# Performance work log

Hardware: AMD Instinct MI355X
Metric: run time of the kernel (lower is better)

## Reference

```python
import jax, jax.numpy as jnp
import numpy as np

B, S, D, H, HID = 4, 1024, 1024, 16, 4096
DK = D // H
EPS = 1e-6


def _ln(x):
    # LayerNorm without affine, eps=1e-6
    mu = jnp.mean(x, axis=-1, keepdims=True)
    var = jnp.var(x, axis=-1, keepdims=True)
    return (x - mu) / jnp.sqrt(var + EPS)


def _lin(x, W, b):
    # torch Linear convention: W is [out, in]
    y = jnp.einsum('...i,oi->...o', x, W)
    return y + b if b is not None else y


def setup_inputs() -> dict:
    key = jax.random.key(0)
    ks = jax.random.split(key, 16)
    sc = lambda fan_in: 1.0 / np.sqrt(fan_in)
    inp = {
        'x': jax.random.normal(ks[0], (B, S, D), jnp.float32),
        'cond': jax.random.normal(ks[1], (B, 1, D), jnp.float32),
        'Wq': jax.random.normal(ks[2], (D, D), jnp.float32) * sc(D),
        'bq': jnp.zeros((D,), jnp.float32),
        'Wk': jax.random.normal(ks[3], (D, D), jnp.float32) * sc(D),
        'bk': jnp.zeros((D,), jnp.float32),
        'Wv': jax.random.normal(ks[4], (D, D), jnp.float32) * sc(D),
        'bv': jnp.zeros((D,), jnp.float32),
        'Wo': jax.random.normal(ks[5], (D, D), jnp.float32) * sc(D),
        'bo': jnp.zeros((D,), jnp.float32),
        'W1': jax.random.normal(ks[6], (HID, D), jnp.float32) * sc(D),
        'b1': jnp.zeros((HID,), jnp.float32),
        'W2': jax.random.normal(ks[7], (D, HID), jnp.float32) * sc(HID),
        'b2': jnp.zeros((D,), jnp.float32),
        'Wada': jax.random.normal(ks[8], (6 * D, D), jnp.float32) * sc(D),
        'bada': jnp.zeros((6 * D,), jnp.float32),
    }
    return inp


def reference(x, cond, Wq, bq, Wk, bk, Wv, bv, Wo, bo, W1, b1, W2, b2, Wada, bada):
    # adaLN modulation: SiLU -> Linear -> chunk 6 along last dim
    mod = _lin(jax.nn.silu(cond), Wada, bada)  # [B,1,6D]
    gama1, beta1, alpha1, gama2, beta2, alpha2 = jnp.split(mod, 6, axis=-1)

    # attention branch
    residual = x
    h = _ln(x) * (1.0 + beta1) + gama1  # modulate(shift=gama1, scale=beta1)
    q = _lin(h, Wq, bq).reshape(B, S, H, DK)
    k = _lin(h, Wk, bk).reshape(B, S, H, DK)
    v = _lin(h, Wv, bv).reshape(B, S, H, DK)
    scores = jnp.einsum('bqhd,bkhd->bhqk', q, k) / jnp.sqrt(jnp.float32(DK))
    probs = jax.nn.softmax(scores, axis=-1)
    attn = jnp.einsum('bhqk,bkhd->bqhd', probs, v).reshape(B, S, D)
    attn = _lin(attn, Wo, bo)
    x = residual + alpha1 * attn

    # MLP branch
    residual = x
    h = _ln(x) * (1.0 + beta2) + gama2
    h = _lin(h, W1, b1)
    h = jax.nn.gelu(h, approximate=False)  # torch nn.GELU default (erf)
    h = _lin(h, W2, b2)
    return residual + alpha2 * h
```

## Files before the change

### kernel.cpp

```cpp
#include <hip/hip_runtime.h>
#include <cstdint>

typedef __bf16 bf16_t;
typedef __bf16 bf16x4 __attribute__((ext_vector_type(4)));
typedef __bf16 bf16x8 __attribute__((ext_vector_type(8)));
typedef float f32x4 __attribute__((ext_vector_type(4)));

#define B_ 4
#define S_ 1024
#define D_ 1024
#define HID_ 4096
#define MEG (1u << 20)

static const size_t OFF_WBF  = 0;
static const size_t OFF_BQKV = 25165824;
static const size_t OFF_MOD  = 25178112;
static const size_t OFF_H    = 25276416;
static const size_t OFF_QKV  = 33665024;
static const size_t OFF_VT   = 58830848;
static const size_t OFF_ATTN = 67219456;
static const size_t OFF_X1   = 75608064;
static const size_t OFF_PART = 92385280;
static const size_t OFF_MLPH = 159494144;

__device__ __forceinline__ void async_copy16(const bf16_t* g, bf16_t* l) {
  __builtin_amdgcn_global_load_lds(
      (__attribute__((address_space(1))) void*)(g),
      (__attribute__((address_space(3))) void*)(l), 16, 0, 0);
}

__global__ __launch_bounds__(256) void convert_pack(
    const float* __restrict__ Wq, const float* __restrict__ Wk,
    const float* __restrict__ Wv, const float* __restrict__ Wo,
    const float* __restrict__ W1, const float* __restrict__ W2,
    const float* __restrict__ bq, const float* __restrict__ bk,
    const float* __restrict__ bv, bf16_t* __restrict__ wbf,
    float* __restrict__ bqkv) {
  const int y = blockIdx.y;
  if (y == 6) {
    int i = blockIdx.x * 256 + threadIdx.x;
    if (i < 3072)
      bqkv[i] = i < 1024 ? bq[i] : (i < 2048 ? bk[i - 1024] : bv[i - 2048]);
    return;
  }
  const float* src; bf16_t* dst; int n;
  switch (y) {
    case 0: src = Wq; dst = wbf;           n = MEG;     break;
    case 1: src = Wk; dst = wbf + MEG;     n = MEG;     break;
    case 2: src = Wv; dst = wbf + 2*MEG;   n = MEG;     break;
    case 3: src = Wo; dst = wbf + 3*MEG;   n = MEG;     break;
    case 4: src = W1; dst = wbf + 4*MEG;   n = 4*MEG;   break;
    default: src = W2; dst = wbf + 8*MEG;  n = 4*MEG;   break;
  }
  int idx = (blockIdx.x * 256 + threadIdx.x) * 4;
  if (idx < n) {
    float4 v = *(const float4*)(src + idx);
    bf16x4 pk;
    pk.x = (__bf16)v.x; pk.y = (__bf16)v.y; pk.z = (__bf16)v.z; pk.w = (__bf16)v.w;
    *(bf16x4*)(dst + idx) = pk;
  }
}

__global__ __launch_bounds__(256) void ada_mod(
    const float* __restrict__ cond, const float* __restrict__ Wada,
    const float* __restrict__ bada, float* __restrict__ mod) {
  const int wave = threadIdx.x >> 6, lane = threadIdx.x & 63;
  const int o = blockIdx.x * 4 + wave;
  const float* wr = Wada + (size_t)o * D_;
  float a0 = 0.f, a1 = 0.f, a2 = 0.f, a3 = 0.f;
#pragma unroll
  for (int l = 0; l < 16; l++) {
    int i = l * 64 + lane;
    float w = wr[i];
    float c0 = cond[i], c1 = cond[1024 + i], c2 = cond[2048 + i], c3 = cond[3072 + i];
    a0 += w * (c0 / (1.0f + __expf(-c0)));
    a1 += w * (c1 / (1.0f + __expf(-c1)));
    a2 += w * (c2 / (1.0f + __expf(-c2)));
    a3 += w * (c3 / (1.0f + __expf(-c3)));
  }
#pragma unroll
  for (int offs = 32; offs; offs >>= 1) {
    a0 += __shfl_xor(a0, offs);
    a1 += __shfl_xor(a1, offs);
    a2 += __shfl_xor(a2, offs);
    a3 += __shfl_xor(a3, offs);
  }
  if (lane == 0) {
    float bb = bada[o];
    mod[o]          = a0 + bb;
    mod[6144 + o]   = a1 + bb;
    mod[12288 + o]  = a2 + bb;
    mod[18432 + o]  = a3 + bb;
  }
}

__global__ __launch_bounds__(256) void ln_modulate(
    const float* __restrict__ X, const float* __restrict__ mod,
    bf16_t* __restrict__ H, int goff) {
  const int row = blockIdx.x;
  const int b = row >> 10;
  const int t = threadIdx.x;
  const float* xr = X + (size_t)row * D_;
  float4 xv = *(const float4*)(xr + t * 4);
  float s = xv.x + xv.y + xv.z + xv.w;
  float q = xv.x*xv.x + xv.y*xv.y + xv.z*xv.z + xv.w*xv.w;
  const int wave = t >> 6, lane = t & 63;
#pragma unroll
  for (int offs = 32; offs; offs >>= 1) {
    s += __shfl_down(s, offs);
    q += __shfl_down(q, offs);
  }
  __shared__ float sb[4][2];
  if (lane == 0) { sb[wave][0] = s; sb[wave][1] = q; }
  __syncthreads();
  float st = sb[0][0] + sb[1][0] + sb[2][0] + sb[3][0];
  float qt = sb[0][1] + sb[1][1] + sb[2][1] + sb[3][1];
  float mu = st * (1.0f / D_);
  float var = qt * (1.0f / D_) - mu * mu;
  float rstd = rsqrtf(var + 1e-6f);
  const float* mb = mod + (size_t)b * 6144 + goff;
  const int c = t * 4;
  float4 gm = *(const float4*)(mb + c);
  float4 bt = *(const float4*)(mb + 1024 + c);
  bf16x4 pk;
  pk.x = (__bf16)((xv.x - mu) * rstd * (1.0f + bt.x) + gm.x);
  pk.y = (__bf16)((xv.y - mu) * rstd * (1.0f + bt.y) + gm.y);
  pk.z = (__bf16)((xv.z - mu) * rstd * (1.0f + bt.z) + gm.z);
  pk.w = (__bf16)((xv.w - mu) * rstd * (1.0f + bt.w) + gm.w);
  *(bf16x4*)(H + (size_t)row * D_ + c) = pk;
}

__global__ __launch_bounds__(256) void transpose_v(
    const bf16_t* __restrict__ qkv, bf16_t* __restrict__ vT) {
  __shared__ bf16_t tile[64][65];
  const int bh = blockIdx.y;
  const int b = bh >> 4, hh = bh & 15;
  const int s0 = blockIdx.x * 64;
  const int t = threadIdx.x;
  const int tx = t & 63, ty = t >> 6;
  const bf16_t* src = qkv + (size_t)b * S_ * 3072 + 2048 + hh * 64;
  for (int r = ty; r < 64; r += 4)
    tile[r][tx] = src[(size_t)(s0 + r) * 3072 + tx];
  __syncthreads();
  bf16_t* dst = vT + (size_t)bh * 64 * 1024;
  for (int r = ty; r < 64; r += 4)
    dst[(size_t)r * 1024 + s0 + tx] = tile[tx][r];
}

__global__ __launch_bounds__(256) void flash_attn(
    const bf16_t* __restrict__ qkv, const bf16_t* __restrict__ vT,
    bf16_t* __restrict__ attn) {
  __shared__ __align__(16) bf16_t Ks[2][2][64 * 64];
  __shared__ __align__(16) bf16_t Vs[2][2][64 * 64];
  __shared__ __align__(16) bf16_t Ps[4][2][16 * 64];

  const int t = threadIdx.x;
  const int wave = t >> 6, lane = t & 63;
  const int lm = lane & 15, quad = lane >> 4;
  const int bh = blockIdx.y;
  const int b = bh >> 4, hh = bh & 15;
  const int s0 = blockIdx.x * 64;

  const bf16_t* qbase = qkv + (size_t)b * S_ * 3072 + hh * 64;
  const bf16_t* kbase = qbase + 1024;
  const bf16_t* vbase = vT + (size_t)bh * (64 * 1024);

  const int row0 = t >> 3;
  const int cg = (t & 7) ^ (row0 & 7);
  const int o0 = t * 8, o1 = 2048 + t * 8;
  const bf16_t* kr = kbase + (size_t)row0 * 3072 + cg * 8;
  const bf16_t* vr0 = vbase + (size_t)row0 * 1024 + cg * 8;
  const bf16_t* vr1 = vbase + (size_t)(32 + row0) * 1024 + cg * 8;

  async_copy16(qbase + (size_t)(s0 + row0) * 3072 + cg * 8, &Ks[1][0][o0]);
  async_copy16(qbase + (size_t)(s0 + 32 + row0) * 3072 + cg * 8, &Ks[1][0][o1]);
  async_copy16(kr, &Ks[0][0][o0]);
  async_copy16(kr + (size_t)32 * 3072, &Ks[0][0][o1]);
  async_copy16(kr + (size_t)64 * 3072, &Ks[0][1][o0]);
  async_copy16(kr + (size_t)96 * 3072, &Ks[0][1][o1]);
  async_copy16(vr0, &Vs[0][0][o0]);
  async_copy16(vr1, &Vs[0][0][o1]);
  async_copy16(vr0 + 64, &Vs[0][1][o0]);
  async_copy16(vr1 + 64, &Vs[0][1][o1]);
  __syncthreads();

  bf16x8 aq0, aq1;
  {
    const int rq = wave * 16 + lm;
    const int rbq = lm & 7;
    aq0 = *(const bf16x8*)&Ks[1][0][rq * 64 + (quad ^ rbq) * 8];
    aq1 = *(const bf16x8*)&Ks[1][0][rq * 64 + ((4 + quad) ^ rbq) * 8];
  }
  __syncthreads();

  f32x4 accO[4] = {};
  float mrow[4], lrow[4];
#pragma unroll
  for (int r = 0; r < 4; r++) { mrow[r] = -1e30f; lrow[r] = 0.f; }

  const float SC = 0.18033688f;
  const int rb = lm & 7;

  for (int tt = 0; tt < 8; ++tt) {
    const int cur = tt & 1;
    if (tt < 7) {
      const int nb = cur ^ 1;
      const size_t k0n = (size_t)(tt + 1) << 7;
      const bf16_t* kn = kr + k0n * 3072;
      async_copy16(kn, &Ks[nb][0][o0]);
      async_copy16(kn + (size_t)32 * 3072, &Ks[nb][0][o1]);
      async_copy16(kn + (size_t)64 * 3072, &Ks[nb][1][o0]);
      async_copy16(kn + (size_t)96 * 3072, &Ks[nb][1][o1]);
      async_copy16(vr0 + k0n, &Vs[nb][0][o0]);
      async_copy16(vr1 + k0n, &Vs[nb][0][o1]);
      async_copy16(vr0 + k0n + 64, &Vs[nb][1][o0]);
      async_copy16(vr1 + k0n + 64, &Vs[nb][1][o1]);
    }

    f32x4 accS[8];
#pragma unroll
    for (int j = 0; j < 8; j++) accS[j] = (f32x4){0.f, 0.f, 0.f, 0.f};
    __builtin_amdgcn_s_setprio(1);
#pragma unroll
    for (int h = 0; h < 2; h++) {
#pragma unroll
      for (int ni = 0; ni < 4; ni++) {
        const int rk = ni * 16 + lm;
        bf16x8 b0 = *(const bf16x8*)&Ks[cur][h][rk * 64 + ((quad ^ rb)) * 8];
        bf16x8 b1 = *(const bf16x8*)&Ks[cur][h][rk * 64 + (((4 + quad) ^ rb)) * 8];
        f32x4 a = accS[h * 4 + ni];
        a = __builtin_amdgcn_mfma_f32_16x16x32_bf16(aq0, b0, a, 0, 0, 0);
        a = __builtin_amdgcn_mfma_f32_16x16x32_bf16(aq1, b1, a, 0, 0, 0);
        accS[h * 4 + ni] = a;
      }
    }
    __builtin_amdgcn_s_setprio(0);

    float mx[4];
#pragma unroll
    for (int r = 0; r < 4; r++) {
      float m0 = fmaxf(fmaxf(accS[0][r], accS[1][r]), fmaxf(accS[2][r], accS[3][r]));
      float m1 = fmaxf(fmaxf(accS[4][r], accS[5][r]), fmaxf(accS[6][r], accS[7][r]));
      float m8 = fmaxf(m0, m1);
      m8 = fmaxf(m8, __shfl_xor(m8, 1));
      m8 = fmaxf(m8, __shfl_xor(m8, 2));
      m8 = fmaxf(m8, __shfl_xor(m8, 4));
      m8 = fmaxf(m8, __shfl_xor(m8, 8));
      mx[r] = m8 * SC;
    }
    bool ok = (mx[0] - mrow[0] <= 8.0f) && (mx[1] - mrow[1] <= 8.0f) &&
              (mx[2] - mrow[2] <= 8.0f) && (mx[3] - mrow[3] <= 8.0f);
    if (!__all(ok)) {
#pragma unroll
      for (int r = 0; r < 4; r++) {
        float mnew = fmaxf(mrow[r], mx[r]);
        float al = exp2f(mrow[r] - mnew);
        mrow[r] = mnew;
        lrow[r] *= al;
#pragma unroll
        for (int di = 0; di < 4; di++) accO[di][r] *= al;
      }
    }
#pragma unroll
    for (int r = 0; r < 4; r++) {
      float sum = 0.f;
#pragma unroll
      for (int j = 0; j < 8; j++) {
        float p = exp2f(accS[j][r] * SC - mrow[r]);
        accS[j][r] = p;
        sum += p;
      }
      sum += __shfl_xor(sum, 1);
      sum += __shfl_xor(sum, 2);
      sum += __shfl_xor(sum, 4);
      sum += __shfl_xor(sum, 8);
      lrow[r] += sum;
    }

#pragma unroll
    for (int j = 0; j < 8; j++)
#pragma unroll
      for (int r = 0; r < 4; r++) {
        int prow = quad * 4 + r;
        int c = (j & 3) * 16 + lm;
        Ps[wave][j >> 2][prow * 64 + (((c >> 3) ^ (prow & 7)) << 3) + (c & 7)] =
            (__bf16)accS[j][r];
      }

    __builtin_amdgcn_s_setprio(1);
#pragma unroll
    for (int ks = 0; ks < 4; ks++) {
      const int half = ks >> 1, loc = ks & 1;
      bf16x8 ap = *(const bf16x8*)&Ps[wave][half]
          [lm * 64 + (((loc * 4 + quad) ^ rb)) * 8];
#pragma unroll
      for (int di = 0; di < 4; di++) {
        const int rv = di * 16 + lm;
        bf16x8 vv = *(const bf16x8*)&Vs[cur][half]
            [rv * 64 + (((loc * 4 + quad) ^ rb)) * 8];
        accO[di] = __builtin_amdgcn_mfma_f32_16x16x32_bf16(ap, vv, accO[di], 0, 0, 0);
      }
    }
    __builtin_amdgcn_s_setprio(0);
    __syncthreads();
  }

#pragma unroll
  for (int r = 0; r < 4; r++) {
    float inv = 1.0f / lrow[r];
    int prow = quad * 4 + r;
#pragma unroll
    for (int di = 0; di < 4; di++) {
      int col = di * 16 + lm;
      int cph = (col >> 3) ^ (prow & 7);
      Ps[wave][0][prow * 64 + cph * 8 + (col & 7)] = (__bf16)(accO[di][r] * inv);
    }
  }
  bf16_t* abase = attn + (size_t)b * S_ * 1024 +
                  (size_t)(s0 + wave * 16) * 1024 + hh * 64;
#pragma unroll
  for (int it = 0; it < 2; it++) {
    int slot = it * 64 + lane;
    int orow = slot >> 3;
    int gc = slot & 7;
    int cph = gc ^ (orow & 7);
    bf16x8 val = *(const bf16x8*)&Ps[wave][0][orow * 64 + cph * 8];
    *(bf16x8*)(abase + (size_t)orow * 1024 + gc * 8) = val;
  }
}

template <int EPI>
__global__ __launch_bounds__(256) void gemm_bt(
    const bf16_t* __restrict__ A, int lda, long long sAz,
    const bf16_t* __restrict__ B, int ldb, long long sBz,
    void* __restrict__ Cv, int ldc, long long sCz,
    int M, int N, int K,
    const float* __restrict__ bias,
    float scale) {
  __shared__ __align__(16) bf16_t As[2][128 * 32];
  __shared__ __align__(16) bf16_t Bs[2][128 * 32];

  const int z = blockIdx.z;
  A += (size_t)z * sAz;
  B += (size_t)z * sBz;

  {
    int d = blockIdx.x + gridDim.x * blockIdx.y;
    int xcd = d & 7, sId = d >> 3;
    int qq = sId & 31, panel = sId >> 5;
    const int bx = panel * 8 + (qq >> 2);
    const int by = xcd * 4 + (qq & 3);
    const int t = threadIdx.x;
    const int wave = t >> 6;
    const int lane = t & 63;
    const int lm = lane & 15;
    const int quad = lane >> 4;
    const int wr = wave >> 1;
    const int wc = wave & 1;

    const int m0 = by * 128;
    const int n0 = bx * 128;

    f32x4 acc[4][4] = {};

    const int srow = t >> 2;
    const int gch = (t & 3) ^ ((srow >> 1) & 3);
    const int lds_off = t * 8;
    const bf16_t* Ap0 = A + (size_t)(m0 + srow) * lda + gch * 8;
    const bf16_t* Ap1 = A + (size_t)(m0 + 64 + srow) * lda + gch * 8;
    const bf16_t* Bp0 = B + (size_t)(n0 + srow) * ldb + gch * 8;
    const bf16_t* Bp1 = B + (size_t)(n0 + 64 + srow) * ldb + gch * 8;

    const int sOff = (quad ^ ((lm >> 1) & 3)) * 8;

    const int niter = K >> 5;
    async_copy16(Ap0, &As[0][lds_off]);
    async_copy16(Ap1, &As[0][2048 + lds_off]);
    async_copy16(Bp0, &Bs[0][lds_off]);
    async_copy16(Bp1, &Bs[0][2048 + lds_off]);

    for (int it = 0; it < niter; ++it) {
      asm volatile("s_waitcnt vmcnt(0)\n\ts_barrier" ::: "memory");
      if (it + 1 < niter) {
        const int ko = (it + 1) << 5;
        const int nb = (it + 1) & 1;
        async_copy16(Ap0 + ko, &As[nb][lds_off]);
        async_copy16(Ap1 + ko, &As[nb][2048 + lds_off]);
        async_copy16(Bp0 + ko, &Bs[nb][lds_off]);
        async_copy16(Bp1 + ko, &Bs[nb][2048 + lds_off]);
      }
      const int cb = it & 1;
      bf16x8 af[4], bfr[4];
#pragma unroll
      for (int i = 0; i < 4; i++) {
        af[i] = *(const bf16x8*)&As[cb][(wr * 64 + i * 16 + lm) * 32 + sOff];
        bfr[i] = *(const bf16x8*)&Bs[cb][(wc * 64 + i * 16 + lm) * 32 + sOff];
      }
#pragma unroll
      for (int mi = 0; mi < 4; mi++)
#pragma unroll
        for (int ni = 0; ni < 4; ni++)
          acc[mi][ni] = __builtin_amdgcn_mfma_f32_16x16x32_bf16(
              af[mi], bfr[ni], acc[mi][ni], 0, 0, 0);
    }

    const size_t cz = (size_t)z * sCz;
#pragma unroll
    for (int mi = 0; mi < 4; mi++) {
#pragma unroll
      for (int ni = 0; ni < 4; ni++) {
#pragma unroll
        for (int r = 0; r < 4; r++) {
          int row = m0 + wr * 64 + mi * 16 + quad * 4 + r;
          int col = n0 + wc * 64 + ni * 16 + lm;
          float v = acc[mi][ni][r];
          size_t idx = cz + (size_t)row * ldc + col;
          if (EPI == 1) {
            ((float*)Cv)[idx] = v * scale;
          } else if (EPI == 0) {
            if (bias) v += bias[col];
            ((bf16_t*)Cv)[idx] = (__bf16)v;
          } else if (EPI == 3) {
            v += bias[col];
            float u = 1.5957691216f * (v + 0.044715f * v * v * v);
            float g = v / (1.0f + __expf(-u));
            ((bf16_t*)Cv)[idx] = (__bf16)g;
          }
        }
      }
    }
  }
}

__global__ __launch_bounds__(256) void reduce_ln(
    const float* __restrict__ part, const float* __restrict__ x,
    const float* __restrict__ bo, const float* __restrict__ mod,
    float* __restrict__ x1, bf16_t* __restrict__ h) {
  const int row = blockIdx.x;
  const int b = row >> 10;
  const int t = threadIdx.x;
  const int c = t * 4;
  const size_t idx = (size_t)row * 1024 + c;
  float4 p0 = *(const float4*)(part + idx);
  float4 p1 = *(const float4*)(part + 4194304 + idx);
  float4 bb = *(const float4*)(bo + c);
  float4 al = *(const float4*)(mod + (size_t)b * 6144 + 2048 + c);
  float4 xs = *(const float4*)(x + idx);
  float4 xv;
  xv.x = xs.x + al.x * (p0.x + p1.x + bb.x);
  xv.y = xs.y + al.y * (p0.y + p1.y + bb.y);
  xv.z = xs.z + al.z * (p0.z + p1.z + bb.z);
  xv.w = xs.w + al.w * (p0.w + p1.w + bb.w);
  *(float4*)(x1 + idx) = xv;

  float s = xv.x + xv.y + xv.z + xv.w;
  float q = xv.x*xv.x + xv.y*xv.y + xv.z*xv.z + xv.w*xv.w;
  const int wave = t >> 6, lane = t & 63;
#pragma unroll
  for (int offs = 32; offs; offs >>= 1) {
    s += __shfl_down(s, offs);
    q += __shfl_down(q, offs);
  }
  __shared__ float sb[4][2];
  if (lane == 0) { sb[wave][0] = s; sb[wave][1] = q; }
  __syncthreads();
  float st = sb[0][0] + sb[1][0] + sb[2][0] + sb[3][0];
  float qt = sb[0][1] + sb[1][1] + sb[2][1] + sb[3][1];
  float mu = st * (1.0f / D_);
  float var = qt * (1.0f / D_) - mu * mu;
  float rstd = rsqrtf(var + 1e-6f);
  const float* mb = mod + (size_t)b * 6144 + 3072;
  float4 gm = *(const float4*)(mb + c);
  float4 bt = *(const float4*)(mb + 1024 + c);
  bf16x4 pk;
  pk.x = (__bf16)((xv.x - mu) * rstd * (1.0f + bt.x) + gm.x);
  pk.y = (__bf16)((xv.y - mu) * rstd * (1.0f + bt.y) + gm.y);
  pk.z = (__bf16)((xv.z - mu) * rstd * (1.0f + bt.z) + gm.z);
  pk.w = (__bf16)((xv.w - mu) * rstd * (1.0f + bt.w) + gm.w);
  *(bf16x4*)(h + idx) = pk;
}

__global__ __launch_bounds__(256) void reduce_w2(
    const float* __restrict__ part, const float* __restrict__ x1,
    const float* __restrict__ b2, const float* __restrict__ mod,
    float* __restrict__ out) {
  const int idx = (blockIdx.x * 256 + threadIdx.x) * 4;
  const int col = idx & 1023;
  const int row = idx >> 10;
  const int b = row >> 10;
  float4 s0 = *(const float4*)(part + idx);
  float4 s1 = *(const float4*)(part + 4194304 + idx);
  float4 bb = *(const float4*)(b2 + col);
  float4 al = *(const float4*)(mod + (size_t)b * 6144 + 5120 + col);
  float4 rs = *(const float4*)(x1 + idx);
  float4 o;
  o.x = rs.x + al.x * (s0.x + s1.x + bb.x);
  o.y = rs.y + al.y * (s0.y + s1.y + bb.y);
  o.z = rs.z + al.z * (s0.z + s1.z + bb.z);
  o.w = rs.w + al.w * (s0.w + s1.w + bb.w);
  *(float4*)(out + idx) = o;
}

extern "C" void kernel_launch(void* const* d_in, const int* in_sizes, int n_in,
                              void* d_out, int out_size, void* d_ws, size_t ws_size,
                              hipStream_t stream) {
  (void)in_sizes; (void)n_in; (void)out_size; (void)ws_size;
  const float* x    = (const float*)d_in[0];
  const float* cond = (const float*)d_in[1];
  const float* Wq   = (const float*)d_in[2];
  const float* bq   = (const float*)d_in[3];
  const float* Wk   = (const float*)d_in[4];
  const float* bk   = (const float*)d_in[5];
  const float* Wv   = (const float*)d_in[6];
  const float* bv   = (const float*)d_in[7];
  const float* Wo   = (const float*)d_in[8];
  const float* bo   = (const float*)d_in[9];
  const float* W1   = (const float*)d_in[10];
  const float* b1   = (const float*)d_in[11];
  const float* W2   = (const float*)d_in[12];
  const float* b2   = (const float*)d_in[13];
  const float* Wada = (const float*)d_in[14];
  const float* bada = (const float*)d_in[15];

  uint8_t* ws = (uint8_t*)d_ws;
  bf16_t* wbf   = (bf16_t*)(ws + OFF_WBF);
  float*  bqkv  = (float*)(ws + OFF_BQKV);
  float*  mod   = (float*)(ws + OFF_MOD);
  bf16_t* h     = (bf16_t*)(ws + OFF_H);
  bf16_t* qkv   = (bf16_t*)(ws + OFF_QKV);
  bf16_t* vT    = (bf16_t*)(ws + OFF_VT);
  bf16_t* attn  = (bf16_t*)(ws + OFF_ATTN);
  float*  x1    = (float*)(ws + OFF_X1);
  float*  part  = (float*)(ws + OFF_PART);
  bf16_t* mlph  = (bf16_t*)(ws + OFF_MLPH);
  float* out = (float*)d_out;

  convert_pack<<<dim3(4096, 7, 1), 256, 0, stream>>>(Wq, Wk, Wv, Wo, W1, W2,
                                                     bq, bk, bv, wbf, bqkv);
  ada_mod<<<1536, 256, 0, stream>>>(cond, Wada, bada, mod);
  ln_modulate<<<4096, 256, 0, stream>>>(x, mod, h, 0);
  gemm_bt<0><<<dim3(24, 32, 1), 256, 0, stream>>>(
      h, 1024, 0, wbf, 1024, 0, qkv, 3072, 0, 4096, 3072, 1024,
      bqkv, 1.f);
  transpose_v<<<dim3(16, 64, 1), 256, 0, stream>>>(qkv, vT);
  flash_attn<<<dim3(16, 64, 1), 256, 0, stream>>>(qkv, vT, attn);

  gemm_bt<1><<<dim3(8, 32, 2), 256, 0, stream>>>(
      attn, 1024, 512, wbf + (size_t)3 * MEG, 1024, 512, part, 1024, 4194304,
      4096, 1024, 512, nullptr, 1.f);
  reduce_ln<<<4096, 256, 0, stream>>>(part, x, bo, mod, x1, h);

  gemm_bt<3><<<dim3(32, 32, 1), 256, 0, stream>>>(
      h, 1024, 0, wbf + (size_t)4 * MEG, 1024, 0, mlph, 4096, 0,
      4096, 4096, 1024, b1, 1.f);
  gemm_bt<1><<<dim3(8, 32, 2), 256, 0, stream>>>(
      mlph, 4096, 2048, wbf + (size_t)8 * MEG, 4096, 2048, part, 1024, 4194304,
      4096, 1024, 2048, nullptr, 1.f);
  reduce_w2<<<4096, 256, 0, stream>>>(part, x1, b2, mod, out);
}
```

Before: 404.4 us.

## Use 512-thread flash-attention blocks with 128 queries sharing each K/V tile

Flash attention now runs 8 waves per block covering 128 query rows instead of 4 waves covering 64, so each K/V tile loaded into LDS is reused by twice as many queries and global K/V traffic per query is halved. Each thread issues fewer async copies per tile. The P buffer is shrunk to one 16x64 slice per wave and the PV product is done in two halves. The row-sum shuffle reduction is deferred to the end instead of running every iteration. The costs are fewer blocks in the grid (512 instead of 1024) and a larger block with a launch-bounds occupancy hint, which may hurt latency hiding.

Result: faster. 393.1 us (-2.8%).

```diff
diff --git a/kernel.cpp b/kernel.cpp
--- a/kernel.cpp
+++ b/kernel.cpp
@@ -147,19 +147,19 @@
     dst[(size_t)r * 1024 + s0 + tx] = tile[tx][r];
 }
 
-__global__ __launch_bounds__(256) void flash_attn(
+__global__ __launch_bounds__(512, 4) void flash_attn(
     const bf16_t* __restrict__ qkv, const bf16_t* __restrict__ vT,
     bf16_t* __restrict__ attn) {
   __shared__ __align__(16) bf16_t Ks[2][2][64 * 64];
   __shared__ __align__(16) bf16_t Vs[2][2][64 * 64];
-  __shared__ __align__(16) bf16_t Ps[4][2][16 * 64];
+  __shared__ __align__(16) bf16_t Ps[8][16 * 64];
 
   const int t = threadIdx.x;
   const int wave = t >> 6, lane = t & 63;
   const int lm = lane & 15, quad = lane >> 4;
   const int bh = blockIdx.y;
   const int b = bh >> 4, hh = bh & 15;
-  const int s0 = blockIdx.x * 64;
+  const int s0 = blockIdx.x * 128;
 
   const bf16_t* qbase = qkv + (size_t)b * S_ * 3072 + hh * 64;
   const bf16_t* kbase = qbase + 1024;
@@ -167,54 +167,44 @@
 
   const int row0 = t >> 3;
   const int cg = (t & 7) ^ (row0 & 7);
-  const int o0 = t * 8, o1 = 2048 + t * 8;
-  const bf16_t* kr = kbase + (size_t)row0 * 3072 + cg * 8;
-  const bf16_t* vr0 = vbase + (size_t)row0 * 1024 + cg * 8;
-  const bf16_t* vr1 = vbase + (size_t)(32 + row0) * 1024 + cg * 8;
-
-  async_copy16(qbase + (size_t)(s0 + row0) * 3072 + cg * 8, &Ks[1][0][o0]);
-  async_copy16(qbase + (size_t)(s0 + 32 + row0) * 3072 + cg * 8, &Ks[1][0][o1]);
-  async_copy16(kr, &Ks[0][0][o0]);
-  async_copy16(kr + (size_t)32 * 3072, &Ks[0][0][o1]);
-  async_copy16(kr + (size_t)64 * 3072, &Ks[0][1][o0]);
-  async_copy16(kr + (size_t)96 * 3072, &Ks[0][1][o1]);
-  async_copy16(vr0, &Vs[0][0][o0]);
-  async_copy16(vr1, &Vs[0][0][o1]);
-  async_copy16(vr0 + 64, &Vs[0][1][o0]);
-  async_copy16(vr1 + 64, &Vs[0][1][o1]);
+  const int od = t * 8;
+
+  async_copy16(qbase + (size_t)(s0 + row0) * 3072 + cg * 8, &Ks[1][0][od]);
+  async_copy16(qbase + (size_t)(s0 + 64 + row0) * 3072 + cg * 8, &Ks[1][1][od]);
+  async_copy16(kbase + (size_t)row0 * 3072 + cg * 8, &Ks[0][0][od]);
+  async_copy16(kbase + (size_t)(64 + row0) * 3072 + cg * 8, &Ks[0][1][od]);
+  async_copy16(vbase + (size_t)row0 * 1024 + cg * 8, &Vs[0][0][od]);
+  async_copy16(vbase + (size_t)row0 * 1024 + 64 + cg * 8, &Vs[0][1][od]);
   __syncthreads();
 
   bf16x8 aq0, aq1;
   {
     const int rq = wave * 16 + lm;
+    const int qh = rq >> 6, qr = rq & 63;
     const int rbq = lm & 7;
-    aq0 = *(const bf16x8*)&Ks[1][0][rq * 64 + (quad ^ rbq) * 8];
-    aq1 = *(const bf16x8*)&Ks[1][0][rq * 64 + ((4 + quad) ^ rbq) * 8];
+    aq0 = *(const bf16x8*)&Ks[1][qh][qr * 64 + (quad ^ rbq) * 8];
+    aq1 = *(const bf16x8*)&Ks[1][qh][qr * 64 + ((4 + quad) ^ rbq) * 8];
   }
   __syncthreads();
 
   f32x4 accO[4] = {};
-  float mrow[4], lrow[4];
-#pragma unroll
-  for (int r = 0; r < 4; r++) { mrow[r] = -1e30f; lrow[r] = 0.f; }
+  float mrow[4], lsum[4];
+#pragma unroll
+  for (int r = 0; r < 4; r++) { mrow[r] = -1e30f; lsum[r] = 0.f; }
 
   const float SC = 0.18033688f;
   const int rb = lm & 7;
+  bf16_t* Pw = Ps[wave];
 
   for (int tt = 0; tt < 8; ++tt) {
     const int cur = tt & 1;
     if (tt < 7) {
       const int nb = cur ^ 1;
       const size_t k0n = (size_t)(tt + 1) << 7;
-      const bf16_t* kn = kr + k0n * 3072;
-      async_copy16(kn, &Ks[nb][0][o0]);
-      async_copy16(kn + (size_t)32 * 3072, &Ks[nb][0][o1]);
-      async_copy16(kn + (size_t)64 * 3072, &Ks[nb][1][o0]);
-      async_copy16(kn + (size_t)96 * 3072, &Ks[nb][1][o1]);
-      async_copy16(vr0 + k0n, &Vs[nb][0][o0]);
-      async_copy16(vr1 + k0n, &Vs[nb][0][o1]);
-      async_copy16(vr0 + k0n + 64, &Vs[nb][1][o0]);
-      async_copy16(vr1 + k0n + 64, &Vs[nb][1][o1]);
+      async_copy16(kbase + (k0n + row0) * 3072 + cg * 8, &Ks[nb][0][od]);
+      async_copy16(kbase + (k0n + 64 + row0) * 3072 + cg * 8, &Ks[nb][1][od]);
+      async_copy16(vbase + (size_t)row0 * 1024 + k0n + cg * 8, &Vs[nb][0][od]);
+      async_copy16(vbase + (size_t)row0 * 1024 + k0n + 64 + cg * 8, &Vs[nb][1][od]);
     }
 
     f32x4 accS[8];
@@ -222,16 +212,16 @@
     for (int j = 0; j < 8; j++) accS[j] = (f32x4){0.f, 0.f, 0.f, 0.f};
     __builtin_amdgcn_s_setprio(1);
 #pragma unroll
-    for (int h = 0; h < 2; h++) {
+    for (int hf = 0; hf < 2; hf++) {
 #pragma unroll
       for (int ni = 0; ni < 4; ni++) {
         const int rk = ni * 16 + lm;
-        bf16x8 b0 = *(const bf16x8*)&Ks[cur][h][rk * 64 + ((quad ^ rb)) * 8];
-        bf16x8 b1 = *(const bf16x8*)&Ks[cur][h][rk * 64 + (((4 + quad) ^ rb)) * 8];
-        f32x4 a = accS[h * 4 + ni];
+        bf16x8 b0 = *(const bf16x8*)&Ks[cur][hf][rk * 64 + ((quad ^ rb)) * 8];
+        bf16x8 b1 = *(const bf16x8*)&Ks[cur][hf][rk * 64 + (((4 + quad) ^ rb)) * 8];
+        f32x4 a = accS[hf * 4 + ni];
         a = __builtin_amdgcn_mfma_f32_16x16x32_bf16(aq0, b0, a, 0, 0, 0);
         a = __builtin_amdgcn_mfma_f32_16x16x32_bf16(aq1, b1, a, 0, 0, 0);
-        accS[h * 4 + ni] = a;
+        accS[hf * 4 + ni] = a;
       }
     }
     __builtin_amdgcn_s_setprio(0);
@@ -256,7 +246,7 @@
         float mnew = fmaxf(mrow[r], mx[r]);
         float al = exp2f(mrow[r] - mnew);
         mrow[r] = mnew;
-        lrow[r] *= al;
+        lsum[r] *= al;
 #pragma unroll
         for (int di = 0; di < 4; di++) accO[di][r] *= al;
       }
@@ -270,50 +260,56 @@
         accS[j][r] = p;
         sum += p;
       }
-      sum += __shfl_xor(sum, 1);
-      sum += __shfl_xor(sum, 2);
-      sum += __shfl_xor(sum, 4);
-      sum += __shfl_xor(sum, 8);
-      lrow[r] += sum;
-    }
-
-#pragma unroll
-    for (int j = 0; j < 8; j++)
-#pragma unroll
-      for (int r = 0; r < 4; r++) {
-        int prow = quad * 4 + r;
-        int c = (j & 3) * 16 + lm;
-        Ps[wave][j >> 2][prow * 64 + (((c >> 3) ^ (prow & 7)) << 3) + (c & 7)] =
-            (__bf16)accS[j][r];
-      }
-
-    __builtin_amdgcn_s_setprio(1);
-#pragma unroll
-    for (int ks = 0; ks < 4; ks++) {
-      const int half = ks >> 1, loc = ks & 1;
-      bf16x8 ap = *(const bf16x8*)&Ps[wave][half]
-          [lm * 64 + (((loc * 4 + quad) ^ rb)) * 8];
-#pragma unroll
-      for (int di = 0; di < 4; di++) {
-        const int rv = di * 16 + lm;
-        bf16x8 vv = *(const bf16x8*)&Vs[cur][half]
-            [rv * 64 + (((loc * 4 + quad) ^ rb)) * 8];
-        accO[di] = __builtin_amdgcn_mfma_f32_16x16x32_bf16(ap, vv, accO[di], 0, 0, 0);
-      }
-    }
-    __builtin_amdgcn_s_setprio(0);
+      lsum[r] += sum;
+    }
+
+#pragma unroll
+    for (int hf = 0; hf < 2; hf++) {
+#pragma unroll
+      for (int jj = 0; jj < 4; jj++)
+#pragma unroll
+        for (int r = 0; r < 4; r++) {
+          int prow = quad * 4 + r;
+          int c = jj * 16 + lm;
+          Pw[prow * 64 + (((c >> 3) ^ (prow & 7)) << 3) + (c & 7)] =
+              (__bf16)accS[hf * 4 + jj][r];
+        }
+      __builtin_amdgcn_s_setprio(1);
+#pragma unroll
+      for (int loc = 0; loc < 2; loc++) {
+        bf16x8 ap = *(const bf16x8*)&Pw[lm * 64 + (((loc * 4 + quad) ^ rb)) * 8];
+#pragma unroll
+        for (int di = 0; di < 4; di++) {
+          const int rv = di * 16 + lm;
+          bf16x8 vv = *(const bf16x8*)&Vs[cur][hf]
+              [rv * 64 + (((loc * 4 + quad) ^ rb)) * 8];
+          accO[di] = __builtin_amdgcn_mfma_f32_16x16x32_bf16(ap, vv, accO[di], 0, 0, 0);
+        }
+      }
+      __builtin_amdgcn_s_setprio(0);
+    }
     __syncthreads();
   }
 
 #pragma unroll
   for (int r = 0; r < 4; r++) {
-    float inv = 1.0f / lrow[r];
+    float sv = lsum[r];
+    sv += __shfl_xor(sv, 1);
+    sv += __shfl_xor(sv, 2);
+    sv += __shfl_xor(sv, 4);
+    sv += __shfl_xor(sv, 8);
+    lsum[r] = sv;
+  }
+
+#pragma unroll
+  for (int r = 0; r < 4; r++) {
+    float inv = 1.0f / lsum[r];
     int prow = quad * 4 + r;
 #pragma unroll
     for (int di = 0; di < 4; di++) {
       int col = di * 16 + lm;
       int cph = (col >> 3) ^ (prow & 7);
-      Ps[wave][0][prow * 64 + cph * 8 + (col & 7)] = (__bf16)(accO[di][r] * inv);
+      Pw[prow * 64 + cph * 8 + (col & 7)] = (__bf16)(accO[di][r] * inv);
     }
   }
   bf16_t* abase = attn + (size_t)b * S_ * 1024 +
@@ -324,7 +320,7 @@
     int orow = slot >> 3;
     int gc = slot & 7;
     int cph = gc ^ (orow & 7);
-    bf16x8 val = *(const bf16x8*)&Ps[wave][0][orow * 64 + cph * 8];
+    bf16x8 val = *(const bf16x8*)&Pw[orow * 64 + cph * 8];
     *(bf16x8*)(abase + (size_t)orow * 1024 + gc * 8) = val;
   }
 }
@@ -543,7 +539,7 @@
       h, 1024, 0, wbf, 1024, 0, qkv, 3072, 0, 4096, 3072, 1024,
       bqkv, 1.f);
   transpose_v<<<dim3(16, 64, 1), 256, 0, stream>>>(qkv, vT);
-  flash_attn<<<dim3(16, 64, 1), 256, 0, stream>>>(qkv, vT, attn);
+  flash_attn<<<dim3(8, 64, 1), 512, 0, stream>>>(qkv, vT, attn);
 
   gemm_bt<1><<<dim3(8, 32, 2), 256, 0, stream>>>(
       attn, 1024, 512, wbf + (size_t)3 * MEG, 1024, 512, part, 1024, 4194304,
```
